# Kernel tuning notes

Measured on AMD Instinct MI355X. Metric: run time of the kernel, lower is better.

The kernel has to match this reference:

```python
import jax, jax.numpy as jnp
import numpy as np

WINDOW = 7
SHIFT = 3
NUM_HEADS = 12
DIM = 384
FFN = 4 * DIM
EPS = 1e-5


def _rel_pos_index(w):
    coords = np.stack(np.meshgrid(np.arange(w), np.arange(w), indexing='ij'))  # [2,w,w]
    flat = coords.reshape(2, -1)
    rel = (flat[:, :, None] - flat[:, None, :]).transpose(1, 2, 0)  # [w*w, w*w, 2]
    rel[..., 0] += w - 1
    rel[..., 1] += w - 1
    rel[..., 0] *= 2 * w - 1
    return rel.sum(-1).astype(np.int32)  # [w*w, w*w]


def _attn_mask(hp, wp, w, s):
    # replicate get_attn_mask: region labeling, window partition, pairwise diff
    img = np.zeros((hp, wp), dtype=np.float32)
    cnt = 0
    for hs in (slice(0, -w), slice(-w, -s), slice(-s, None)):
        for ws in (slice(0, -w), slice(-w, -s), slice(-s, None)):
            img[hs, ws] = cnt
            cnt += 1
    mw = img.reshape(hp // w, w, wp // w, w).transpose(0, 2, 1, 3).reshape(-1, w * w)
    diff = mw[:, None, :] - mw[:, :, None]  # unsqueeze(1) - unsqueeze(2)
    return jnp.asarray(np.where(diff != 0, -100.0, 0.0).astype(np.float32))


def _ln(x, g, b):
    mu = jnp.mean(x, -1, keepdims=True)
    var = jnp.mean(jnp.square(x - mu), -1, keepdims=True)
    return (x - mu) * jax.lax.rsqrt(var + EPS) * g + b


def setup_inputs() -> dict:
    key = jax.random.key(0)
    ks = jax.random.split(key, 12)
    B, H, W, C = 8, 56, 56, DIM
    sd = 0.02
    inp = {
        'hidden_states': jax.random.normal(ks[0], (B, H * W, C), jnp.float32),
        'ln1_g': jnp.ones((C,), jnp.float32), 'ln1_b': jnp.zeros((C,), jnp.float32),
        'q_w': jax.random.normal(ks[1], (C, C), jnp.float32) * sd, 'q_b': jnp.zeros((C,), jnp.float32),
        'k_w': jax.random.normal(ks[2], (C, C), jnp.float32) * sd, 'k_b': jnp.zeros((C,), jnp.float32),
        'v_w': jax.random.normal(ks[3], (C, C), jnp.float32) * sd, 'v_b': jnp.zeros((C,), jnp.float32),
        'rpb_table': jax.random.normal(ks[4], ((2 * WINDOW - 1) ** 2, NUM_HEADS), jnp.float32) * sd,
        'rp_index': jnp.asarray(_rel_pos_index(WINDOW)),
        'proj_w': jax.random.normal(ks[5], (C, C), jnp.float32) * sd, 'proj_b': jnp.zeros((C,), jnp.float32),
        'ln2_g': jnp.ones((C,), jnp.float32), 'ln2_b': jnp.zeros((C,), jnp.float32),
        'fc1_w': jax.random.normal(ks[6], (C, FFN), jnp.float32) * sd, 'fc1_b': jnp.zeros((FFN,), jnp.float32),
        'fc2_w': jax.random.normal(ks[7], (FFN, C), jnp.float32) * sd, 'fc2_b': jnp.zeros((C,), jnp.float32),
        'height': H, 'width': W,
    }
    return inp


def reference(hidden_states, ln1_g, ln1_b, q_w, q_b, k_w, k_b, v_w, v_b,
              rpb_table, rp_index, proj_w, proj_b, ln2_g, ln2_b,
              fc1_w, fc1_b, fc2_w, fc2_b, height, width):
    w, s, nh = WINDOW, SHIFT, NUM_HEADS
    B, L, C = hidden_states.shape
    hd = C // nh
    shortcut = hidden_states

    x = _ln(hidden_states, ln1_g, ln1_b).reshape(B, height, width, C)
    pad_b = (w - height % w) % w
    pad_r = (w - width % w) % w
    if pad_b or pad_r:
        x = jnp.pad(x, ((0, 0), (0, pad_b), (0, pad_r), (0, 0)))
    Hp, Wp = height + pad_b, width + pad_r

    if s > 0:
        x = jnp.roll(x, shift=(-s, -s), axis=(1, 2))

    # window partition -> [B*nW, w*w, C]
    N = w * w
    xw = x.reshape(B, Hp // w, w, Wp // w, w, C).transpose(0, 1, 3, 2, 4, 5).reshape(-1, N, C)

    q = (xw @ q_w + q_b).reshape(-1, N, nh, hd).transpose(0, 2, 1, 3)
    k = (xw @ k_w + k_b).reshape(-1, N, nh, hd).transpose(0, 2, 1, 3)
    v = (xw @ v_w + v_b).reshape(-1, N, nh, hd).transpose(0, 2, 1, 3)

    scores = jnp.einsum('whnd,whmd->whnm', q, k) / jnp.sqrt(jnp.float32(hd))
    bias = rpb_table[rp_index.reshape(-1)].reshape(N, N, nh).transpose(2, 0, 1)
    scores = scores + bias[None]

    if s > 0:
        mask = _attn_mask(Hp, Wp, w, s)  # [nW, N, N]
        nW = mask.shape[0]
        scores = scores.reshape(B, nW, nh, N, N) + mask[None, :, None]
        scores = scores.reshape(-1, nh, N, N)

    probs = jax.nn.softmax(scores, axis=-1)
    ctx = jnp.einsum('whnm,whmd->whnd', probs, v).transpose(0, 2, 1, 3).reshape(-1, N, C)
    attn_out = ctx @ proj_w + proj_b

    # window reverse
    xr = attn_out.reshape(B, Hp // w, Wp // w, w, w, C).transpose(0, 1, 3, 2, 4, 5).reshape(B, Hp, Wp, C)
    if s > 0:
        xr = jnp.roll(xr, shift=(s, s), axis=(1, 2))
    if pad_b or pad_r:
        xr = xr[:, :height, :width, :]
    xr = xr.reshape(B, height * width, C)

    h = shortcut + xr
    y = _ln(h, ln2_g, ln2_b)
    y = jax.nn.gelu(y @ fc1_w + fc1_b, approximate=False)
    return h + (y @ fc2_w + fc2_b)
```

## Files before the change

### kernel.cpp

```cpp
#include <hip/hip_runtime.h>
#include <hip/hip_bf16.h>

typedef unsigned short u16;
typedef short bf16x8 __attribute__((ext_vector_type(8)));
typedef float f32x4 __attribute__((ext_vector_type(4)));

__device__ __forceinline__ u16 f2bf(float x) {
  __hip_bfloat16 h = __float2bfloat16(x);
  return *reinterpret_cast<u16*>(&h);
}
__device__ __forceinline__ float bf2f(u16 x) {
  __hip_bfloat16 h = *reinterpret_cast<__hip_bfloat16*>(&x);
  return __bfloat162float(h);
}
__device__ __forceinline__ float rdany(const void* p, size_t i, int f) {
  return f ? ((const float*)p)[i] : bf2f(((const u16*)p)[i]);
}

__device__ __forceinline__ float gelu_fast(float x) {
  float x2 = x * x;
  float u2 = 1.5957691216057308f * x * __builtin_fmaf(0.044715f, x2, 1.f);
  float e = __expf(u2);
  float r = 1.f / (e + 1.f);
  return x - x * r;
}

__global__ void detect_k(const u16* __restrict__ ln1g_raw, int* __restrict__ flag) {
  if (threadIdx.x == 0 && blockIdx.x == 0)
    *flag = (ln1g_raw[0] == 0 && ln1g_raw[2] == 0) ? 1 : 0;
}

__global__ __launch_bounds__(256) void prep_k(
    const void* qw, const void* kw, const void* vw, const void* pw,
    const void* f1w, const void* f2w,
    u16* __restrict__ qwT, u16* __restrict__ kwT, u16* __restrict__ vwT,
    u16* __restrict__ pwT, u16* __restrict__ f1T, u16* __restrict__ f2T,
    const void* s0, const void* s1, const void* s2, const void* s3,
    const void* s4, const void* s5, const void* s6, const void* s7,
    const void* s8, const void* s9, const void* s10,
    u16* __restrict__ vecdst, const int* __restrict__ rpi,
    u16* __restrict__ biasT, const int* __restrict__ flag) {
  int f = *flag;
  int b = blockIdx.x;
  if (b >= 1728) {
    int tid = threadIdx.y * 32 + threadIdx.x;
    if (b == 1729) {
      for (int i = tid; i < 28812; i += 256) {
        int hh = i / 2401, r = i - hh * 2401;
        biasT[i] = f2bf(rdany(s10, (size_t)rpi[r] * 12 + hh, f));
      }
      return;
    }
    const void* srcs[11] = {s0, s1, s2, s3, s4, s5, s6, s7, s8, s9, s10};
    const int offs[12] = {0, 384, 768, 1152, 1536, 1920, 2304, 2688, 3072, 3456, 4992, 7020};
    for (int i = tid; i < 7020; i += 256) {
      int seg = 0;
#pragma unroll
      for (int t = 1; t < 11; t++) seg += (i >= offs[t]) ? 1 : 0;
      vecdst[i] = f2bf(rdany(srcs[seg], i - offs[seg], f));
    }
    return;
  }
  const void* src; u16* dst; int R, C, bx, by;
  if (b < 576) {
    int m = b / 144, t = b - m * 144;
    src = (m == 0) ? qw : (m == 1) ? kw : (m == 2) ? vw : pw;
    dst = (m == 0) ? qwT : (m == 1) ? kwT : (m == 2) ? vwT : pwT;
    R = 384; C = 384; bx = t % 12; by = t / 12;
  } else if (b < 1152) {
    int t = b - 576; src = f1w; dst = f1T; R = 384; C = 1536;
    bx = t % 48; by = t / 48;
  } else {
    int t = b - 1152; src = f2w; dst = f2T; R = 1536; C = 384;
    bx = t % 12; by = t / 12;
  }
  __shared__ u16 tbuf[32][33];
  int x = threadIdx.x, y = threadIdx.y;
  int gx = bx * 32, gy = by * 32;
#pragma unroll
  for (int j = 0; j < 32; j += 8)
    tbuf[y + j][x] = f2bf(rdany(src, (size_t)(gy + y + j) * C + gx + x, f));
  __syncthreads();
#pragma unroll
  for (int j = 0; j < 32; j += 8) dst[(size_t)(gx + y + j) * R + gy + x] = tbuf[x][y + j];
}

__global__ __launch_bounds__(256) void ln1_window_k(
    const void* __restrict__ hid, const u16* __restrict__ g,
    const u16* __restrict__ b, u16* __restrict__ xw, int rowoff,
    const int* __restrict__ flag) {
  int f = *flag;
  int wv = threadIdx.x >> 6, lane = threadIdx.x & 63;
  int lrow = blockIdx.x * 4 + wv;
  int row = rowoff + lrow;
  int wid = row / 49, n = row - wid * 49;
  int bimg = wid >> 6, w8 = wid & 63;
  int wi = w8 >> 3, wj = w8 & 7;
  int p = n / 7, q = n - p * 7;
  int si = wi * 7 + p + 3; if (si >= 56) si -= 56;
  int sj = wj * 7 + q + 3; if (sj >= 56) sj -= 56;
  size_t src = ((size_t)bimg * 3136 + si * 56 + sj) * 384;
  float x[6]; float s = 0.f, s2 = 0.f;
#pragma unroll
  for (int e = 0; e < 6; e++) {
    x[e] = rdany(hid, src + e * 64 + lane, f);
    s += x[e]; s2 += x[e] * x[e];
  }
#pragma unroll
  for (int off = 32; off; off >>= 1) { s += __shfl_xor(s, off); s2 += __shfl_xor(s2, off); }
  float mu = s * (1.f / 384.f);
  float var = s2 * (1.f / 384.f) - mu * mu;
  float rs = 1.f / sqrtf(var + 1e-5f);
  size_t dst = (size_t)lrow * 384;
#pragma unroll
  for (int e = 0; e < 6; e++) {
    int c = e * 64 + lane;
    float yv = (x[e] - mu) * rs * bf2f(g[c]) + bf2f(b[c]);
    xw[dst + c] = f2bf(yv);
  }
}

__global__ __launch_bounds__(256) void ln2_k(
    const float* hsrc, const u16* __restrict__ g,
    const u16* __restrict__ b, u16* __restrict__ out) {
  int wv = threadIdx.x >> 6, lane = threadIdx.x & 63;
  int row = blockIdx.x * 4 + wv;
  size_t src = (size_t)row * 384;
  float x[6]; float s = 0.f, s2 = 0.f;
#pragma unroll
  for (int e = 0; e < 6; e++) {
    x[e] = hsrc[src + e * 64 + lane];
    s += x[e]; s2 += x[e] * x[e];
  }
#pragma unroll
  for (int off = 32; off; off >>= 1) { s += __shfl_xor(s, off); s2 += __shfl_xor(s2, off); }
  float mu = s * (1.f / 384.f);
  float var = s2 * (1.f / 384.f) - mu * mu;
  float rs = 1.f / sqrtf(var + 1e-5f);
#pragma unroll
  for (int e = 0; e < 6; e++) {
    int c = e * 64 + lane;
    float yv = (x[e] - mu) * rs * bf2f(g[c]) + bf2f(b[c]);
    out[src + c] = f2bf(yv);
  }
}

template <int EPI>
__global__ __launch_bounds__(256, 4) void gemm_bt(
    const u16* __restrict__ A, const u16* __restrict__ Bt,
    const u16* __restrict__ bias, void* outB,
    const void* __restrict__ shortcut, const float* hres,
    int M, int N, int K, int gmoff, int gx, const int* __restrict__ flag) {
  __shared__ __align__(16) u16 As[2][128 * 36];
  __shared__ __align__(16) u16 Bs[2][128 * 36];
  int bx = blockIdx.x;
  if (bx >= gx) return;
  int tid = threadIdx.x;
  int m0 = bx * 128, n0 = blockIdx.y * 128;
  int lane = tid & 63, wv = tid >> 6;
  int wm = (wv >> 1) * 64, wn = (wv & 1) * 64;
  int l15 = lane & 15, quad = lane >> 4;
  f32x4 acc[4][4];
#pragma unroll
  for (int a = 0; a < 4; a++)
#pragma unroll
    for (int c = 0; c < 4; c++) acc[a][c] = (f32x4){0.f, 0.f, 0.f, 0.f};

  int rowS[2], cS[2], ldsW[2];
#pragma unroll
  for (int i = 0; i < 2; i++) {
    int id = i * 256 + tid;
    rowS[i] = id >> 2;
    cS[i] = id & 3;
    ldsW[i] = rowS[i] * 36 + cS[i] * 8;
  }
  const u16* pA[2]; const u16* pB[2];
#pragma unroll
  for (int i = 0; i < 2; i++) {
    pA[i] = A + (size_t)(m0 + rowS[i]) * K + cS[i] * 8;
    pB[i] = Bt + (size_t)(n0 + rowS[i]) * K + cS[i] * 8;
  }

  uint4 ra[2], rb[2];
#pragma unroll
  for (int i = 0; i < 2; i++) { ra[i] = *(const uint4*)pA[i]; rb[i] = *(const uint4*)pB[i]; }
#pragma unroll
  for (int i = 0; i < 2; i++) { pA[i] += 32; pB[i] += 32; }
#pragma unroll
  for (int i = 0; i < 2; i++) {
    *(uint2*)&As[0][ldsW[i]] = make_uint2(ra[i].x, ra[i].y);
    *(uint2*)&As[0][ldsW[i] + 4] = make_uint2(ra[i].z, ra[i].w);
    *(uint2*)&Bs[0][ldsW[i]] = make_uint2(rb[i].x, rb[i].y);
    *(uint2*)&Bs[0][ldsW[i] + 4] = make_uint2(rb[i].z, rb[i].w);
  }
  __syncthreads();

  int cur = 0;
  for (int kb = 0; kb < K; kb += 32) {
    bool more = (kb + 32 < K);
    if (more) {
#pragma unroll
      for (int i = 0; i < 2; i++) { ra[i] = *(const uint4*)pA[i]; rb[i] = *(const uint4*)pB[i]; }
#pragma unroll
      for (int i = 0; i < 2; i++) { pA[i] += 32; pB[i] += 32; }
    }
    __builtin_amdgcn_sched_barrier(0);
    __builtin_amdgcn_s_setprio(1);
    {
      bf16x8 af[4], bfv[4];
#pragma unroll
      for (int mi = 0; mi < 4; mi++) {
        int base = (wm + mi * 16 + l15) * 36 + quad * 8;
        union { uint2 h[2]; bf16x8 v; } u;
        u.h[0] = *(const uint2*)&As[cur][base];
        u.h[1] = *(const uint2*)&As[cur][base + 4];
        af[mi] = u.v;
      }
#pragma unroll
      for (int ni = 0; ni < 4; ni++) {
        int base = (wn + ni * 16 + l15) * 36 + quad * 8;
        union { uint2 h[2]; bf16x8 v; } u;
        u.h[0] = *(const uint2*)&Bs[cur][base];
        u.h[1] = *(const uint2*)&Bs[cur][base + 4];
        bfv[ni] = u.v;
      }
#pragma unroll
      for (int mi = 0; mi < 4; mi++)
#pragma unroll
        for (int ni = 0; ni < 4; ni++)
          acc[mi][ni] = __builtin_amdgcn_mfma_f32_16x16x32_bf16(af[mi], bfv[ni], acc[mi][ni], 0, 0, 0);
    }
    __builtin_amdgcn_s_setprio(0);
    __builtin_amdgcn_sched_barrier(0);
    __syncthreads();
    if (more) {
#pragma unroll
      for (int i = 0; i < 2; i++) {
        *(uint2*)&As[cur ^ 1][ldsW[i]] = make_uint2(ra[i].x, ra[i].y);
        *(uint2*)&As[cur ^ 1][ldsW[i] + 4] = make_uint2(ra[i].z, ra[i].w);
        *(uint2*)&Bs[cur ^ 1][ldsW[i]] = make_uint2(rb[i].x, rb[i].y);
        *(uint2*)&Bs[cur ^ 1][ldsW[i] + 4] = make_uint2(rb[i].z, rb[i].w);
      }
    }
    __syncthreads();
    cur ^= 1;
  }

  int f = (EPI == 2) ? *flag : 0;
  float biasv[4];
#pragma unroll
  for (int ni = 0; ni < 4; ni++) biasv[ni] = bf2f(bias[n0 + wn + ni * 16 + l15]);
  int seg = n0 / 384;
#pragma unroll
  for (int mi = 0; mi < 4; mi++) {
#pragma unroll
    for (int r = 0; r < 4; r++) {
      int gm = m0 + wm + mi * 16 + quad * 4 + r;
      size_t orow = 0;
      if (EPI == 2) {
        int grow = gmoff + gm;
        int wid = grow / 49, nIn = grow - wid * 49;
        int bimg = wid >> 6, w8 = wid & 63;
        int wi = w8 >> 3, wj = w8 & 7;
        int p = nIn / 7, q = nIn - p * 7;
        int oi = wi * 7 + p + 3; if (oi >= 56) oi -= 56;
        int oj = wj * 7 + q + 3; if (oj >= 56) oj -= 56;
        orow = ((size_t)bimg * 3136 + oi * 56 + oj) * 384;
      }
#pragma unroll
      for (int ni = 0; ni < 4; ni++) {
        int gn = n0 + wn + ni * 16 + l15;
        float v = acc[mi][ni][r] + biasv[ni];
        if (EPI == 1) {
          v = gelu_fast(v);
          ((u16*)outB)[(size_t)gm * N + gn] = f2bf(v);
        } else if (EPI == 2) {
          float hv = rdany(shortcut, orow + gn, f) + v;
          hv = fminf(fmaxf(hv, -1000.f), 1000.f);
          ((float*)outB)[orow + gn] = hv;
        } else if (EPI == 3) {
          float t = v + hres[(size_t)gm * N + gn];
          t = fminf(fmaxf(t, -1000.f), 1000.f);
          ((float*)outB)[(size_t)gm * N + gn] = t;
        } else {
          u16* dst = (u16*)outB + (size_t)seg * M * 384;
          dst[(size_t)gm * 384 + (gn - seg * 384)] = f2bf(v);
        }
      }
    }
  }
}

__global__ __launch_bounds__(256, 5) void attn_k(
    const u16* __restrict__ Q, const u16* __restrict__ Kb, const u16* __restrict__ V,
    const u16* __restrict__ biasT, u16* __restrict__ ctx, int wdoff) {
  __shared__ __align__(16) u16 qs[64 * 56];
  __shared__ __align__(16) u16 ks_[64 * 56];
  __shared__ __align__(16) u16 vt[32 * 72];
  __shared__ __align__(16) u16 P[64 * 72];
  __shared__ int regid[49];
  int lwd = blockIdx.x, hh = blockIdx.y;
  int wd = wdoff + lwd;
  int tid = threadIdx.x;
  int w8 = wd & 63, wi = w8 >> 3, wj = w8 & 7;

  for (int idx = tid; idx < 840; idx += 256) {
    int rr = idx / 56, cc = idx - rr * 56;
    qs[(49 + rr) * 56 + cc] = 0;
    ks_[(49 + rr) * 56 + cc] = 0;
  }
  for (int idx = tid; idx < 480; idx += 256) {
    int d = idx / 15, m = 49 + (idx - d * 15);
    vt[d * 72 + m] = 0;
  }
  if (tid < 49) {
    int p = tid / 7, q = tid - p * 7;
    int rr = (wi == 7) ? (p < 4 ? 1 : 2) : 0;
    int cc = (wj == 7) ? (q < 4 ? 1 : 2) : 0;
    regid[tid] = rr * 3 + cc;
  }
  size_t base = ((size_t)lwd * 49) * 384 + hh * 32;
  for (int idx = tid; idx < 392; idx += 256) {
    int mat = idx >= 196;
    int rid = idx - mat * 196;
    int n = rid >> 2, c = rid & 3;
    uint4 val = *(const uint4*)((mat ? Kb : Q) + base + (size_t)n * 384 + c * 8);
    *(uint4*)&((mat ? ks_ : qs)[n * 56 + c * 8]) = val;
  }
  for (int idx = tid; idx < 196; idx += 256) {
    int n = idx >> 2, c = idx & 3;
    uint4 val = *(const uint4*)(V + base + (size_t)n * 384 + c * 8);
    u16 tmp[8];
    *(uint4*)tmp = val;
#pragma unroll
    for (int t = 0; t < 8; t++) vt[(c * 8 + t) * 72 + n] = tmp[t];
  }
  __syncthreads();

  int lane = tid & 63, wv = tid >> 6, l15 = lane & 15, quad = lane >> 4;
  f32x4 zero = (f32x4){0.f, 0.f, 0.f, 0.f};
  bf16x8 aq = *(const bf16x8*)&qs[(wv * 16 + l15) * 56 + quad * 8];
  f32x4 sc[4];
#pragma unroll
  for (int mi = 0; mi < 4; mi++) {
    bf16x8 bk = *(const bf16x8*)&ks_[(mi * 16 + l15) * 56 + quad * 8];
    sc[mi] = __builtin_amdgcn_mfma_f32_16x16x32_bf16(aq, bk, zero, 0, 0, 0);
  }
  const float scale = 0.17677669529663687f;

  int rm[4];
#pragma unroll
  for (int mi = 0; mi < 4; mi++) {
    int m = mi * 16 + l15;
    rm[mi] = (m < 49) ? regid[m] : -2;
  }
  float pv[4][4];
#pragma unroll
  for (int r = 0; r < 4; r++) {
    int n = wv * 16 + quad * 4 + r;
    int rn = (n < 49) ? regid[n] : -1;
    const u16* brow = biasT + hh * 2401 + n * 49;
#pragma unroll
    for (int mi = 0; mi < 4; mi++) {
      int m = mi * 16 + l15;
      float v = sc[mi][r] * scale;
      if (n < 49 && m < 49) {
        v += bf2f(brow[m]);
        if (rn != rm[mi]) v -= 100.f;
      }
      if (m >= 49) v = -1e4f;
      pv[r][mi] = v;
    }
    float mx = fmaxf(fmaxf(pv[r][0], pv[r][1]), fmaxf(pv[r][2], pv[r][3]));
#pragma unroll
    for (int off = 1; off < 16; off <<= 1) mx = fmaxf(mx, __shfl_xor(mx, off));
    float sum = 0.f;
#pragma unroll
    for (int mi = 0; mi < 4; mi++) {
      pv[r][mi] = __expf(pv[r][mi] - mx);
      sum += pv[r][mi];
    }
#pragma unroll
    for (int off = 1; off < 16; off <<= 1) sum += __shfl_xor(sum, off);
    float inv = 1.f / sum;
#pragma unroll
    for (int mi = 0; mi < 4; mi++)
      P[n * 72 + mi * 16 + l15] = f2bf(pv[r][mi] * inv);
  }

  f32x4 oacc[2]; oacc[0] = zero; oacc[1] = zero;
#pragma unroll
  for (int ks = 0; ks < 2; ks++) {
    bf16x8 ap = *(const bf16x8*)&P[(wv * 16 + l15) * 72 + ks * 32 + quad * 8];
#pragma unroll
    for (int ni = 0; ni < 2; ni++) {
      bf16x8 bv = *(const bf16x8*)&vt[(ni * 16 + l15) * 72 + ks * 32 + quad * 8];
      oacc[ni] = __builtin_amdgcn_mfma_f32_16x16x32_bf16(ap, bv, oacc[ni], 0, 0, 0);
    }
  }
#pragma unroll
  for (int ni = 0; ni < 2; ni++) {
#pragma unroll
    for (int r = 0; r < 4; r++) {
      int n = wv * 16 + quad * 4 + r;
      if (n < 49) {
        int d = ni * 16 + l15;
        ctx[base + (size_t)n * 384 + d] = f2bf(oacc[ni][r]);
      }
    }
  }
}

static inline int pad8(int gx) { return (gx + 7) & ~7; }

extern "C" void kernel_launch(void* const* d_in, const int* in_sizes, int n_in,
                              void* d_out, int out_size, void* d_ws, size_t ws_size,
                              hipStream_t stream) {
  const void* hid = d_in[0];
  const void* ln1g = d_in[1];
  const void* ln1b = d_in[2];
  const void* qw = d_in[3];
  const void* qb = d_in[4];
  const void* kw = d_in[5];
  const void* kbias = d_in[6];
  const void* vw = d_in[7];
  const void* vb = d_in[8];
  const void* rpb = d_in[9];
  const int* rpi = (const int*)d_in[10];
  const void* pw = d_in[11];
  const void* pb = d_in[12];
  const void* ln2g = d_in[13];
  const void* ln2b = d_in[14];
  const void* f1w = d_in[15];
  const void* f1b = d_in[16];
  const void* f2w = d_in[17];
  const void* f2b = d_in[18];

  char* ws = (char*)d_ws;
  u16* wT = (u16*)ws;
  u16* qwT = wT;
  u16* kwT = qwT + 147456;
  u16* vwT = kwT + 147456;
  u16* pwT = vwT + 147456;
  u16* f1T = pwT + 147456;
  u16* f2T = f1T + 589824;
  u16* VEC = (u16*)(ws + 3538944);
  u16* s_ln1g = VEC + 0;
  u16* s_ln1b = VEC + 384;
  u16* s_qkvb = VEC + 768;
  u16* s_pb = VEC + 1920;
  u16* s_ln2g = VEC + 2304;
  u16* s_ln2b = VEC + 2688;
  u16* s_f2b = VEC + 3072;
  u16* s_f1b = VEC + 3456;
  u16* s_rpb = VEC + 4992;
  int* flag = (int*)(ws + 3552984);
  u16* biasT = (u16*)(ws + 3552992);
  const size_t head = 3610624;

  size_t avail = (ws_size > head) ? ws_size - head : 0;
  int rows1 = (avail >= (size_t)25088 * 3072) ? 25088
            : (avail >= (size_t)12544 * 3072) ? 12544 : 6272;
  int rows2 = (avail >= (size_t)25088 * 3840) ? 25088
            : (avail >= (size_t)12544 * 3840) ? 12544 : 3584;

  u16* P1 = (u16*)(ws + head);
  u16* xw = P1;
  u16* Qb = P1 + (size_t)rows1 * 384;
  u16* Kb = Qb + (size_t)rows1 * 384;
  u16* Vb = Kb + (size_t)rows1 * 384;
  u16* y2 = P1;
  u16* f1o = P1 + (size_t)rows2 * 384;
  float* hbuf = (float*)d_out;

  detect_k<<<1, 64, 0, stream>>>((const u16*)ln1g, flag);
  dim3 tb(32, 8);
  prep_k<<<1730, tb, 0, stream>>>(qw, kw, vw, pw, f1w, f2w,
                                  qwT, kwT, vwT, pwT, f1T, f2T,
                                  ln1g, ln1b, qb, kbias, vb, pb, ln2g, ln2b,
                                  f2b, f1b, rpb, VEC, rpi, biasT, flag);

  for (int off = 0; off < 25088; off += rows1) {
    int gx = rows1 / 128;
    ln1_window_k<<<rows1 / 4, 256, 0, stream>>>(hid, s_ln1g, s_ln1b, xw, off, flag);
    gemm_bt<4><<<dim3(pad8(gx), 9), 256, 0, stream>>>(
        xw, qwT, s_qkvb, Qb, nullptr, nullptr, rows1, 1152, 384, 0, gx, flag);
    attn_k<<<dim3(rows1 / 49, 12), 256, 0, stream>>>(Qb, Kb, Vb, biasT, xw, off / 49);
    gemm_bt<2><<<dim3(pad8(gx), 3), 256, 0, stream>>>(
        xw, pwT, s_pb, hbuf, hid, nullptr, rows1, 384, 384, off, gx, flag);
  }

  for (int off = 0; off < 25088; off += rows2) {
    int gx = rows2 / 128;
    ln2_k<<<rows2 / 4, 256, 0, stream>>>(hbuf + (size_t)off * 384, s_ln2g, s_ln2b, y2);
    gemm_bt<1><<<dim3(pad8(gx), 12), 256, 0, stream>>>(
        y2, f1T, s_f1b, f1o, nullptr, nullptr, rows2, 1536, 384, 0, gx, flag);
    gemm_bt<3><<<dim3(pad8(gx), 3), 256, 0, stream>>>(
        f1o, f2T, s_f2b, hbuf + (size_t)off * 384, nullptr,
        hbuf + (size_t)off * 384, rows2, 384, 1536, 0, gx, flag);
  }
}
```

Baseline: 392.1 us.

## Use single-buffered 64-wide K tiles with register prefetch in GEMM

The GEMM K-step grows from 32 to 64, so each iteration runs two MFMA sub-steps per barrier pair. The double-buffered LDS layout is replaced by a single buffer with row stride 68, which keeps LDS at 34 KB. Global loads for the tile after next are issued into registers right after the LDS store, so more latency can be hidden. In exchange, each thread holds twice as many staging registers and there is no LDS double buffering, so compute and the LDS store are serialized by barriers.

After: 476.7 us. 21.6% more time.

```diff
diff --git a/kernel.cpp b/kernel.cpp
--- a/kernel.cpp
+++ b/kernel.cpp
@@ -151,8 +151,8 @@
     const u16* __restrict__ bias, void* outB,
     const void* __restrict__ shortcut, const float* hres,
     int M, int N, int K, int gmoff, int gx, const int* __restrict__ flag) {
-  __shared__ __align__(16) u16 As[2][128 * 36];
-  __shared__ __align__(16) u16 Bs[2][128 * 36];
+  __shared__ __align__(16) u16 As[128 * 68];
+  __shared__ __align__(16) u16 Bs[128 * 68];
   int bx = blockIdx.x;
   if (bx >= gx) return;
   int tid = threadIdx.x;
@@ -166,62 +166,62 @@
 #pragma unroll
     for (int c = 0; c < 4; c++) acc[a][c] = (f32x4){0.f, 0.f, 0.f, 0.f};
 
-  int rowS[2], cS[2], ldsW[2];
-#pragma unroll
-  for (int i = 0; i < 2; i++) {
+  int rowS[4], cS[4], ldsW[4];
+#pragma unroll
+  for (int i = 0; i < 4; i++) {
     int id = i * 256 + tid;
-    rowS[i] = id >> 2;
-    cS[i] = id & 3;
-    ldsW[i] = rowS[i] * 36 + cS[i] * 8;
-  }
-  const u16* pA[2]; const u16* pB[2];
-#pragma unroll
-  for (int i = 0; i < 2; i++) {
+    rowS[i] = id >> 3;
+    cS[i] = id & 7;
+    ldsW[i] = rowS[i] * 68 + cS[i] * 8;
+  }
+  const u16* pA[4]; const u16* pB[4];
+#pragma unroll
+  for (int i = 0; i < 4; i++) {
     pA[i] = A + (size_t)(m0 + rowS[i]) * K + cS[i] * 8;
     pB[i] = Bt + (size_t)(n0 + rowS[i]) * K + cS[i] * 8;
   }
 
-  uint4 ra[2], rb[2];
-#pragma unroll
-  for (int i = 0; i < 2; i++) { ra[i] = *(const uint4*)pA[i]; rb[i] = *(const uint4*)pB[i]; }
-#pragma unroll
-  for (int i = 0; i < 2; i++) { pA[i] += 32; pB[i] += 32; }
-#pragma unroll
-  for (int i = 0; i < 2; i++) {
-    *(uint2*)&As[0][ldsW[i]] = make_uint2(ra[i].x, ra[i].y);
-    *(uint2*)&As[0][ldsW[i] + 4] = make_uint2(ra[i].z, ra[i].w);
-    *(uint2*)&Bs[0][ldsW[i]] = make_uint2(rb[i].x, rb[i].y);
-    *(uint2*)&Bs[0][ldsW[i] + 4] = make_uint2(rb[i].z, rb[i].w);
-  }
-  __syncthreads();
-
-  int cur = 0;
-  for (int kb = 0; kb < K; kb += 32) {
-    bool more = (kb + 32 < K);
-    if (more) {
-#pragma unroll
-      for (int i = 0; i < 2; i++) { ra[i] = *(const uint4*)pA[i]; rb[i] = *(const uint4*)pB[i]; }
-#pragma unroll
-      for (int i = 0; i < 2; i++) { pA[i] += 32; pB[i] += 32; }
-    }
-    __builtin_amdgcn_sched_barrier(0);
+  uint4 ra[4], rb[4];
+#pragma unroll
+  for (int i = 0; i < 4; i++) { ra[i] = *(const uint4*)pA[i]; rb[i] = *(const uint4*)pB[i]; }
+#pragma unroll
+  for (int i = 0; i < 4; i++) { pA[i] += 64; pB[i] += 64; }
+#pragma unroll
+  for (int i = 0; i < 4; i++) {
+    *(uint2*)&As[ldsW[i]] = make_uint2(ra[i].x, ra[i].y);
+    *(uint2*)&As[ldsW[i] + 4] = make_uint2(ra[i].z, ra[i].w);
+    *(uint2*)&Bs[ldsW[i]] = make_uint2(rb[i].x, rb[i].y);
+    *(uint2*)&Bs[ldsW[i] + 4] = make_uint2(rb[i].z, rb[i].w);
+  }
+  if (K > 64) {
+#pragma unroll
+    for (int i = 0; i < 4; i++) { ra[i] = *(const uint4*)pA[i]; rb[i] = *(const uint4*)pB[i]; }
+#pragma unroll
+    for (int i = 0; i < 4; i++) { pA[i] += 64; pB[i] += 64; }
+  }
+  asm volatile("s_waitcnt lgkmcnt(0)" ::: "memory");
+  __builtin_amdgcn_s_barrier();
+  __builtin_amdgcn_sched_barrier(0);
+
+  for (int kb = 0; kb < K; kb += 64) {
     __builtin_amdgcn_s_setprio(1);
-    {
+#pragma unroll
+    for (int ks = 0; ks < 2; ks++) {
       bf16x8 af[4], bfv[4];
 #pragma unroll
       for (int mi = 0; mi < 4; mi++) {
-        int base = (wm + mi * 16 + l15) * 36 + quad * 8;
+        int base = (wm + mi * 16 + l15) * 68 + (ks * 4 + quad) * 8;
         union { uint2 h[2]; bf16x8 v; } u;
-        u.h[0] = *(const uint2*)&As[cur][base];
-        u.h[1] = *(const uint2*)&As[cur][base + 4];
+        u.h[0] = *(const uint2*)&As[base];
+        u.h[1] = *(const uint2*)&As[base + 4];
         af[mi] = u.v;
       }
 #pragma unroll
       for (int ni = 0; ni < 4; ni++) {
-        int base = (wn + ni * 16 + l15) * 36 + quad * 8;
+        int base = (wn + ni * 16 + l15) * 68 + (ks * 4 + quad) * 8;
         union { uint2 h[2]; bf16x8 v; } u;
-        u.h[0] = *(const uint2*)&Bs[cur][base];
-        u.h[1] = *(const uint2*)&Bs[cur][base + 4];
+        u.h[0] = *(const uint2*)&Bs[base];
+        u.h[1] = *(const uint2*)&Bs[base + 4];
         bfv[ni] = u.v;
       }
 #pragma unroll
@@ -232,18 +232,26 @@
     }
     __builtin_amdgcn_s_setprio(0);
     __builtin_amdgcn_sched_barrier(0);
-    __syncthreads();
-    if (more) {
-#pragma unroll
-      for (int i = 0; i < 2; i++) {
-        *(uint2*)&As[cur ^ 1][ldsW[i]] = make_uint2(ra[i].x, ra[i].y);
-        *(uint2*)&As[cur ^ 1][ldsW[i] + 4] = make_uint2(ra[i].z, ra[i].w);
-        *(uint2*)&Bs[cur ^ 1][ldsW[i]] = make_uint2(rb[i].x, rb[i].y);
-        *(uint2*)&Bs[cur ^ 1][ldsW[i] + 4] = make_uint2(rb[i].z, rb[i].w);
-      }
-    }
-    __syncthreads();
-    cur ^= 1;
+    if (kb + 64 < K) {
+      __builtin_amdgcn_s_barrier();
+      __builtin_amdgcn_sched_barrier(0);
+#pragma unroll
+      for (int i = 0; i < 4; i++) {
+        *(uint2*)&As[ldsW[i]] = make_uint2(ra[i].x, ra[i].y);
+        *(uint2*)&As[ldsW[i] + 4] = make_uint2(ra[i].z, ra[i].w);
+        *(uint2*)&Bs[ldsW[i]] = make_uint2(rb[i].x, rb[i].y);
+        *(uint2*)&Bs[ldsW[i] + 4] = make_uint2(rb[i].z, rb[i].w);
+      }
+      if (kb + 128 < K) {
+#pragma unroll
+        for (int i = 0; i < 4; i++) { ra[i] = *(const uint4*)pA[i]; rb[i] = *(const uint4*)pB[i]; }
+#pragma unroll
+        for (int i = 0; i < 4; i++) { pA[i] += 64; pB[i] += 64; }
+      }
+      asm volatile("s_waitcnt lgkmcnt(0)" ::: "memory");
+      __builtin_amdgcn_s_barrier();
+      __builtin_amdgcn_sched_barrier(0);
+    }
   }
 
   int f = (EPI == 2) ? *flag : 0;
```

## Fuse LayerNorm application into GEMM A-tile loads using precomputed row stats

Applied to the files above, without the earlier changes.

Replaces the standalone LN1 (with window shift/partition) and LN2 kernels with a small per-row stats kernel. The QKV and FC1 GEMMs now read raw fp32/bf16 activations and apply normalization, gamma and beta while staging A tiles into shared memory. This removes the write and re-read of the normalized bf16 intermediates. In exchange, the GEMM loader does more global traffic (fp32 A plus gamma/beta per step) and more ALU work, and it re-reads each A row once per N-tile column block (9 or 12 times).

After: 828.1 us. 111% more time.

```diff
diff --git a/kernel.cpp b/kernel.cpp
--- a/kernel.cpp
+++ b/kernel.cpp
@@ -28,6 +28,26 @@
 __global__ void detect_k(const u16* __restrict__ ln1g_raw, int* __restrict__ flag) {
   if (threadIdx.x == 0 && blockIdx.x == 0)
     *flag = (ln1g_raw[0] == 0 && ln1g_raw[2] == 0) ? 1 : 0;
+}
+
+__global__ __launch_bounds__(256) void stats_k(
+    const void* __restrict__ src, float2* __restrict__ st, int force32,
+    const int* __restrict__ flag) {
+  int f = force32 ? 1 : *flag;
+  int wv = threadIdx.x >> 6, lane = threadIdx.x & 63;
+  int row = blockIdx.x * 4 + wv;
+  size_t base = (size_t)row * 384;
+  float s = 0.f, s2 = 0.f;
+#pragma unroll
+  for (int e = 0; e < 6; e++) {
+    float x = rdany(src, base + e * 64 + lane, f);
+    s += x; s2 += x * x;
+  }
+#pragma unroll
+  for (int off = 32; off; off >>= 1) { s += __shfl_xor(s, off); s2 += __shfl_xor(s2, off); }
+  float mu = s * (1.f / 384.f);
+  float var = s2 * (1.f / 384.f) - mu * mu;
+  if (lane == 0) st[row] = make_float2(mu, 1.f / sqrtf(var + 1e-5f));
 }
 
 __global__ __launch_bounds__(256) void prep_k(
@@ -85,71 +105,13 @@
   for (int j = 0; j < 32; j += 8) dst[(size_t)(gx + y + j) * R + gy + x] = tbuf[x][y + j];
 }
 
-__global__ __launch_bounds__(256) void ln1_window_k(
-    const void* __restrict__ hid, const u16* __restrict__ g,
-    const u16* __restrict__ b, u16* __restrict__ xw, int rowoff,
-    const int* __restrict__ flag) {
-  int f = *flag;
-  int wv = threadIdx.x >> 6, lane = threadIdx.x & 63;
-  int lrow = blockIdx.x * 4 + wv;
-  int row = rowoff + lrow;
-  int wid = row / 49, n = row - wid * 49;
-  int bimg = wid >> 6, w8 = wid & 63;
-  int wi = w8 >> 3, wj = w8 & 7;
-  int p = n / 7, q = n - p * 7;
-  int si = wi * 7 + p + 3; if (si >= 56) si -= 56;
-  int sj = wj * 7 + q + 3; if (sj >= 56) sj -= 56;
-  size_t src = ((size_t)bimg * 3136 + si * 56 + sj) * 384;
-  float x[6]; float s = 0.f, s2 = 0.f;
-#pragma unroll
-  for (int e = 0; e < 6; e++) {
-    x[e] = rdany(hid, src + e * 64 + lane, f);
-    s += x[e]; s2 += x[e] * x[e];
-  }
-#pragma unroll
-  for (int off = 32; off; off >>= 1) { s += __shfl_xor(s, off); s2 += __shfl_xor(s2, off); }
-  float mu = s * (1.f / 384.f);
-  float var = s2 * (1.f / 384.f) - mu * mu;
-  float rs = 1.f / sqrtf(var + 1e-5f);
-  size_t dst = (size_t)lrow * 384;
-#pragma unroll
-  for (int e = 0; e < 6; e++) {
-    int c = e * 64 + lane;
-    float yv = (x[e] - mu) * rs * bf2f(g[c]) + bf2f(b[c]);
-    xw[dst + c] = f2bf(yv);
-  }
-}
-
-__global__ __launch_bounds__(256) void ln2_k(
-    const float* hsrc, const u16* __restrict__ g,
-    const u16* __restrict__ b, u16* __restrict__ out) {
-  int wv = threadIdx.x >> 6, lane = threadIdx.x & 63;
-  int row = blockIdx.x * 4 + wv;
-  size_t src = (size_t)row * 384;
-  float x[6]; float s = 0.f, s2 = 0.f;
-#pragma unroll
-  for (int e = 0; e < 6; e++) {
-    x[e] = hsrc[src + e * 64 + lane];
-    s += x[e]; s2 += x[e] * x[e];
-  }
-#pragma unroll
-  for (int off = 32; off; off >>= 1) { s += __shfl_xor(s, off); s2 += __shfl_xor(s2, off); }
-  float mu = s * (1.f / 384.f);
-  float var = s2 * (1.f / 384.f) - mu * mu;
-  float rs = 1.f / sqrtf(var + 1e-5f);
-#pragma unroll
-  for (int e = 0; e < 6; e++) {
-    int c = e * 64 + lane;
-    float yv = (x[e] - mu) * rs * bf2f(g[c]) + bf2f(b[c]);
-    out[src + c] = f2bf(yv);
-  }
-}
-
-template <int EPI>
+template <int EPI, int LNA>
 __global__ __launch_bounds__(256, 4) void gemm_bt(
-    const u16* __restrict__ A, const u16* __restrict__ Bt,
+    const void* __restrict__ Asrc, const u16* __restrict__ Bt,
     const u16* __restrict__ bias, void* outB,
     const void* __restrict__ shortcut, const float* hres,
+    const float2* __restrict__ lnstat, const u16* __restrict__ lng,
+    const u16* __restrict__ lnb,
     int M, int N, int K, int gmoff, int gx, const int* __restrict__ flag) {
   __shared__ __align__(16) u16 As[2][128 * 36];
   __shared__ __align__(16) u16 Bs[2][128 * 36];
@@ -160,50 +122,113 @@
   int lane = tid & 63, wv = tid >> 6;
   int wm = (wv >> 1) * 64, wn = (wv & 1) * 64;
   int l15 = lane & 15, quad = lane >> 4;
+  int f32a = (LNA == 1) ? *flag : 1;
   f32x4 acc[4][4];
 #pragma unroll
   for (int a = 0; a < 4; a++)
 #pragma unroll
     for (int c = 0; c < 4; c++) acc[a][c] = (f32x4){0.f, 0.f, 0.f, 0.f};
 
-  int rowS[2], cS[2], ldsW[2];
+  int rowA[2], cA[2], ldsA[2];
+  size_t aOff[2];
+  float muv[2], rsv[2];
 #pragma unroll
   for (int i = 0; i < 2; i++) {
     int id = i * 256 + tid;
-    rowS[i] = id >> 2;
-    cS[i] = id & 3;
-    ldsW[i] = rowS[i] * 36 + cS[i] * 8;
-  }
-  const u16* pA[2]; const u16* pB[2];
+    rowA[i] = id >> 2;
+    int c = id & 3;
+    cA[i] = c * 8;
+    ldsA[i] = rowA[i] * 36 + c * 8;
+    if (LNA == 0) {
+      aOff[i] = (size_t)(m0 + rowA[i]) * K + c * 8;
+    } else if (LNA == 1) {
+      int grow = gmoff + m0 + rowA[i];
+      int wid = grow / 49, n = grow - wid * 49;
+      int bimg = wid >> 6, w8 = wid & 63;
+      int wi = w8 >> 3, wj = w8 & 7;
+      int p = n / 7, q = n - p * 7;
+      int si = wi * 7 + p + 3; if (si >= 56) si -= 56;
+      int sj = wj * 7 + q + 3; if (sj >= 56) sj -= 56;
+      size_t srow = (size_t)bimg * 3136 + si * 56 + sj;
+      aOff[i] = srow * 384 + c * 8;
+      float2 st = lnstat[srow];
+      muv[i] = st.x; rsv[i] = st.y;
+    } else {
+      int r = m0 + rowA[i];
+      aOff[i] = (size_t)r * 384 + c * 8;
+      float2 st = lnstat[r];
+      muv[i] = st.x; rsv[i] = st.y;
+    }
+  }
+  int ldsB[2];
+  const u16* pB[2];
 #pragma unroll
   for (int i = 0; i < 2; i++) {
-    pA[i] = A + (size_t)(m0 + rowS[i]) * K + cS[i] * 8;
-    pB[i] = Bt + (size_t)(n0 + rowS[i]) * K + cS[i] * 8;
-  }
-
-  uint4 ra[2], rb[2];
-#pragma unroll
-  for (int i = 0; i < 2; i++) { ra[i] = *(const uint4*)pA[i]; rb[i] = *(const uint4*)pB[i]; }
-#pragma unroll
-  for (int i = 0; i < 2; i++) { pA[i] += 32; pB[i] += 32; }
-#pragma unroll
-  for (int i = 0; i < 2; i++) {
-    *(uint2*)&As[0][ldsW[i]] = make_uint2(ra[i].x, ra[i].y);
-    *(uint2*)&As[0][ldsW[i] + 4] = make_uint2(ra[i].z, ra[i].w);
-    *(uint2*)&Bs[0][ldsW[i]] = make_uint2(rb[i].x, rb[i].y);
-    *(uint2*)&Bs[0][ldsW[i] + 4] = make_uint2(rb[i].z, rb[i].w);
-  }
+    int id = i * 256 + tid;
+    int row = id >> 2, c = id & 3;
+    ldsB[i] = row * 36 + c * 8;
+    pB[i] = Bt + (size_t)(n0 + row) * K + c * 8;
+  }
+
+  uint4 ra0[2], ra1[2], gq[2], bq[2], rb[2];
+
+#define LOADSTEP(kb_)                                                          \
+  {                                                                            \
+    _Pragma("unroll") for (int i = 0; i < 2; i++) {                            \
+      if (LNA == 0) {                                                          \
+        ra0[i] = *(const uint4*)((const u16*)Asrc + aOff[i] + (kb_));          \
+      } else if (f32a) {                                                       \
+        const float* p = (const float*)Asrc + aOff[i] + (kb_);                 \
+        ra0[i] = *(const uint4*)p;                                             \
+        ra1[i] = *(const uint4*)(p + 4);                                       \
+      } else {                                                                 \
+        ra0[i] = *(const uint4*)((const u16*)Asrc + aOff[i] + (kb_));          \
+      }                                                                        \
+      if (LNA) {                                                               \
+        gq[i] = *(const uint4*)(lng + (kb_) + cA[i]);                          \
+        bq[i] = *(const uint4*)(lnb + (kb_) + cA[i]);                          \
+      }                                                                        \
+      rb[i] = *(const uint4*)pB[i]; pB[i] += 32;                               \
+    }                                                                          \
+  }
+
+#define WRITESTEP(buf)                                                         \
+  {                                                                            \
+    _Pragma("unroll") for (int i = 0; i < 2; i++) {                            \
+      uint4 outv;                                                              \
+      if (LNA == 0) {                                                          \
+        outv = ra0[i];                                                         \
+      } else {                                                                 \
+        u16 tmp[8];                                                            \
+        _Pragma("unroll") for (int e = 0; e < 8; e++) {                        \
+          float xv;                                                            \
+          if (f32a) {                                                          \
+            const uint4& s_ = (e < 4) ? ra0[i] : ra1[i];                       \
+            xv = __uint_as_float(((const unsigned*)&s_)[e & 3]);               \
+          } else {                                                             \
+            xv = bf2f(((const u16*)&ra0[i])[e]);                               \
+          }                                                                    \
+          float gg = bf2f(((const u16*)&gq[i])[e]);                            \
+          float bb = bf2f(((const u16*)&bq[i])[e]);                            \
+          tmp[e] = f2bf(fmaf((xv - muv[i]) * rsv[i], gg, bb));                 \
+        }                                                                      \
+        outv = *(const uint4*)tmp;                                             \
+      }                                                                        \
+      *(uint2*)&As[buf][ldsA[i]] = make_uint2(outv.x, outv.y);                 \
+      *(uint2*)&As[buf][ldsA[i] + 4] = make_uint2(outv.z, outv.w);             \
+      *(uint2*)&Bs[buf][ldsB[i]] = make_uint2(rb[i].x, rb[i].y);               \
+      *(uint2*)&Bs[buf][ldsB[i] + 4] = make_uint2(rb[i].z, rb[i].w);           \
+    }                                                                          \
+  }
+
+  LOADSTEP(0);
+  WRITESTEP(0);
   __syncthreads();
 
   int cur = 0;
   for (int kb = 0; kb < K; kb += 32) {
     bool more = (kb + 32 < K);
-    if (more) {
-#pragma unroll
-      for (int i = 0; i < 2; i++) { ra[i] = *(const uint4*)pA[i]; rb[i] = *(const uint4*)pB[i]; }
-#pragma unroll
-      for (int i = 0; i < 2; i++) { pA[i] += 32; pB[i] += 32; }
-    }
+    if (more) LOADSTEP(kb + 32);
     __builtin_amdgcn_sched_barrier(0);
     __builtin_amdgcn_s_setprio(1);
     {
@@ -233,18 +258,12 @@
     __builtin_amdgcn_s_setprio(0);
     __builtin_amdgcn_sched_barrier(0);
     __syncthreads();
-    if (more) {
-#pragma unroll
-      for (int i = 0; i < 2; i++) {
-        *(uint2*)&As[cur ^ 1][ldsW[i]] = make_uint2(ra[i].x, ra[i].y);
-        *(uint2*)&As[cur ^ 1][ldsW[i] + 4] = make_uint2(ra[i].z, ra[i].w);
-        *(uint2*)&Bs[cur ^ 1][ldsW[i]] = make_uint2(rb[i].x, rb[i].y);
-        *(uint2*)&Bs[cur ^ 1][ldsW[i] + 4] = make_uint2(rb[i].z, rb[i].w);
-      }
-    }
+    if (more) WRITESTEP(cur ^ 1);
     __syncthreads();
     cur ^= 1;
   }
+#undef LOADSTEP
+#undef WRITESTEP
 
   int f = (EPI == 2) ? *flag : 0;
   float biasv[4];
@@ -456,7 +475,9 @@
   u16* s_rpb = VEC + 4992;
   int* flag = (int*)(ws + 3552984);
   u16* biasT = (u16*)(ws + 3552992);
-  const size_t head = 3610624;
+  float2* stat1 = (float2*)(ws + 3610624);
+  float2* stat2 = (float2*)(ws + 3811328);
+  const size_t head = 4012032;
 
   size_t avail = (ws_size > head) ? ws_size - head : 0;
   int rows1 = (avail >= (size_t)25088 * 3072) ? 25088
@@ -469,11 +490,11 @@
   u16* Qb = P1 + (size_t)rows1 * 384;
   u16* Kb = Qb + (size_t)rows1 * 384;
   u16* Vb = Kb + (size_t)rows1 * 384;
-  u16* y2 = P1;
   u16* f1o = P1 + (size_t)rows2 * 384;
   float* hbuf = (float*)d_out;
 
   detect_k<<<1, 64, 0, stream>>>((const u16*)ln1g, flag);
+  stats_k<<<6272, 256, 0, stream>>>(hid, stat1, 0, flag);
   dim3 tb(32, 8);
   prep_k<<<1730, tb, 0, stream>>>(qw, kw, vw, pw, f1w, f2w,
                                   qwT, kwT, vwT, pwT, f1T, f2T,
@@ -482,21 +503,24 @@
 
   for (int off = 0; off < 25088; off += rows1) {
     int gx = rows1 / 128;
-    ln1_window_k<<<rows1 / 4, 256, 0, stream>>>(hid, s_ln1g, s_ln1b, xw, off, flag);
-    gemm_bt<4><<<dim3(pad8(gx), 9), 256, 0, stream>>>(
-        xw, qwT, s_qkvb, Qb, nullptr, nullptr, rows1, 1152, 384, 0, gx, flag);
+    gemm_bt<4, 1><<<dim3(pad8(gx), 9), 256, 0, stream>>>(
+        hid, qwT, s_qkvb, Qb, nullptr, nullptr, stat1, s_ln1g, s_ln1b,
+        rows1, 1152, 384, off, gx, flag);
     attn_k<<<dim3(rows1 / 49, 12), 256, 0, stream>>>(Qb, Kb, Vb, biasT, xw, off / 49);
-    gemm_bt<2><<<dim3(pad8(gx), 3), 256, 0, stream>>>(
-        xw, pwT, s_pb, hbuf, hid, nullptr, rows1, 384, 384, off, gx, flag);
+    gemm_bt<2, 0><<<dim3(pad8(gx), 3), 256, 0, stream>>>(
+        xw, pwT, s_pb, hbuf, hid, nullptr, nullptr, nullptr, nullptr,
+        rows1, 384, 384, off, gx, flag);
   }
 
   for (int off = 0; off < 25088; off += rows2) {
     int gx = rows2 / 128;
-    ln2_k<<<rows2 / 4, 256, 0, stream>>>(hbuf + (size_t)off * 384, s_ln2g, s_ln2b, y2);
-    gemm_bt<1><<<dim3(pad8(gx), 12), 256, 0, stream>>>(
-        y2, f1T, s_f1b, f1o, nullptr, nullptr, rows2, 1536, 384, 0, gx, flag);
-    gemm_bt<3><<<dim3(pad8(gx), 3), 256, 0, stream>>>(
+    stats_k<<<rows2 / 4, 256, 0, stream>>>(hbuf + (size_t)off * 384, stat2, 1, flag);
+    gemm_bt<1, 2><<<dim3(pad8(gx), 12), 256, 0, stream>>>(
+        (const void*)(hbuf + (size_t)off * 384), f1T, s_f1b, f1o,
+        nullptr, nullptr, stat2, s_ln2g, s_ln2b, rows2, 1536, 384, 0, gx, flag);
+    gemm_bt<3, 0><<<dim3(pad8(gx), 3), 256, 0, stream>>>(
         f1o, f2T, s_f2b, hbuf + (size_t)off * 384, nullptr,
-        hbuf + (size_t)off * 384, rows2, 384, 1536, 0, gx, flag);
-  }
-}
+        hbuf + (size_t)off * 384, nullptr, nullptr, nullptr,
+        rows2, 384, 1536, 0, gx, flag);
+  }
+}
```
